# Optimization experiments

Hardware: AMD Instinct MI355X
Metric: run time of the kernel (lower is better)

The kernel has to match this reference:

```python
import jax, jax.numpy as jnp
import numpy as np

N, E, D, K, B = 50000, 600000, 128, 8, 64
E_DIM = 16  # edge_attr feature dim (hard-coded nn.Linear(16, in_dim))


def setup_inputs() -> dict:
    key = jax.random.key(0)
    ks = jax.random.split(key, 10)
    x = jax.random.normal(ks[0], (N, D), dtype=jnp.float32)
    edge_index = jax.random.randint(ks[1], (2, E), 0, N)
    edge_attr = jax.random.normal(ks[2], (E, E_DIM), dtype=jnp.float32)
    # binary pocket membership mask [N, K]
    pkt_mask = (jax.random.uniform(ks[3], (N, K)) < 0.3).astype(jnp.float32)
    batch = jnp.sort(jax.random.randint(ks[4], (N,), 0, B))
    s = 1.0 / np.sqrt(D)
    We = jax.random.normal(ks[5], (E_DIM, D), dtype=jnp.float32) * (1.0 / np.sqrt(E_DIM))
    be = jnp.zeros((D,), jnp.float32)
    W1 = jax.random.normal(ks[6], (D, D), dtype=jnp.float32) * s
    b1 = jnp.zeros((D,), jnp.float32)
    W2 = jax.random.normal(ks[7], (D, D), dtype=jnp.float32) * s
    b2 = jnp.zeros((D,), jnp.float32)
    eps = jnp.zeros((), jnp.float32)  # GINEConv train_eps init 0
    gamma = jnp.ones((D,), jnp.float32)
    beta = jnp.zeros((D,), jnp.float32)
    Wv = jax.random.normal(ks[8], (D, D), dtype=jnp.float32) * s
    bv = jnp.zeros((D,), jnp.float32)
    return {"x": x, "edge_index": edge_index, "edge_attr": edge_attr,
            "pkt_mask": pkt_mask, "batch": batch,
            "We": We, "be": be, "W1": W1, "b1": b1, "W2": W2, "b2": b2,
            "eps": eps, "gamma": gamma, "beta": beta, "Wv": Wv, "bv": bv}


def reference(x, edge_index, edge_attr, pkt_mask, batch,
              We, be, W1, b1, W2, b2, eps, gamma, beta, Wv, bv):
    src, dst = edge_index[0], edge_index[1]
    # edge_lin: [E,16] -> [E,D]
    edge_emb = edge_attr @ We + be
    # GINEConv: message = relu(x_src + edge_emb), scatter-add at dst
    msg = jax.nn.relu(x[src] + edge_emb)
    agg = jax.ops.segment_sum(msg, dst, num_segments=N)
    h = (1.0 + eps) * x + agg
    x_res = jax.nn.relu(h @ W1 + b1) @ W2 + b2  # nn MLP
    # virtual feedback: pocket-wise masked mean pooling per graph
    xw = x_res[:, None, :] * pkt_mask[:, :, None]          # [N,K,D]
    pocket_sum = jax.ops.segment_sum(xw.reshape(N, K * D), batch,
                                     num_segments=B).reshape(B, K, D)
    pocket_count = jax.ops.segment_sum(pkt_mask, batch, num_segments=B)  # [B,K]
    pocket_mean = pocket_sum / (pocket_count[:, :, None] + 1e-9)
    pocket_emb = pocket_mean @ Wv + bv                      # [B,K,D]
    node_pe = pocket_emb[batch]                             # gather -> [N,K,D]
    x_res = x_res + (node_pe * pkt_mask[:, :, None]).sum(axis=1)
    # LayerNorm (eps=1e-5, population variance as in torch)
    mu = x_res.mean(axis=-1, keepdims=True)
    var = ((x_res - mu) ** 2).mean(axis=-1, keepdims=True)
    y = (x_res - mu) / jnp.sqrt(var + 1e-5) * gamma + beta
    # ReLU activation; dropout is identity in eval mode
    return jax.nn.relu(y)
```

## Files before the change

kernel.cpp:

```cpp
#include <hip/hip_runtime.h>
#include <hip/hip_bf16.h>
#include <stdint.h>

#define D 128
#define K 8
#define BGRAPH 64
#define CH 64
#define GRP 4

typedef __attribute__((ext_vector_type(8))) short bf16x8;
typedef __attribute__((ext_vector_type(4))) float f32x4;
typedef __attribute__((ext_vector_type(2))) float f32x2;

__device__ __forceinline__ short f2bf(float f) {
    union { float f; uint32_t u; } v; v.f = f;
    const uint32_t r = (v.u + 0x7fffu + ((v.u >> 16) & 1u)) >> 16;
    return (short)r;
}
__device__ __forceinline__ float bflo(uint32_t u) {
    union { uint32_t u; float f; } v; v.u = u << 16; return v.f;
}
__device__ __forceinline__ float bfhi(uint32_t u) {
    union { uint32_t u; float f; } v; v.u = u & 0xffff0000u; return v.f;
}

__global__ __launch_bounds__(256) void prep_kernel(
    const float* __restrict__ x,
    const float* __restrict__ W1, const float* __restrict__ W2,
    const float* __restrict__ We, const float* __restrict__ be,
    const int* __restrict__ dst,
    __hip_bfloat16* __restrict__ xb,
    short* __restrict__ wb1t, short* __restrict__ wb2t,
    short* __restrict__ webt,
    int* __restrict__ deg,
    int NX, int E, int NBX, int NBW)
{
    const int b = blockIdx.x;
    const int t = threadIdx.x;
    if (b < NBX) {
        const int i = b * 2048 + t * 8;
        if (i + 8 <= NX) {
            const float4 a = *(const float4*)(x + i);
            const float4 c = *(const float4*)(x + i + 4);
            short v[8];
            v[0] = f2bf(a.x); v[1] = f2bf(a.y); v[2] = f2bf(a.z); v[3] = f2bf(a.w);
            v[4] = f2bf(c.x); v[5] = f2bf(c.y); v[6] = f2bf(c.z); v[7] = f2bf(c.w);
            *(uint4*)((short*)xb + i) = *(const uint4*)v;
        }
    } else if (b < NBX + NBW) {
        const int idx = (b - NBX) * 256 + t;
        if (idx < 2 * D * D) {
            const int which = idx >> 14;
            const int rem = idx & 16383;
            const int n = rem >> 7;
            const int k = rem & 127;
            const float* W = which ? W2 : W1;
            short* O = which ? wb2t : wb1t;
            O[n * D + k] = f2bf(W[(size_t)k * D + n]);
        } else {
            const int widx = idx - 2 * D * D;
            const int h = widx >> 12;
            const int c = (widx >> 5) & 127;
            const int k = widx & 31;
            float val = 0.f;
            if (k < 16) val = We[k * D + c];
            else if (k == 16) val = be[c];
            const short hi = f2bf(val);
            short outv;
            if (h == 0) outv = hi;
            else {
                union { uint32_t u; float f; } fh;
                fh.u = ((uint32_t)(unsigned short)hi) << 16;
                outv = f2bf(val - fh.f);
            }
            webt[(h << 12) + c * 32 + k] = outv;
        }
    } else {
        const int i = ((b - NBX - NBW) * 256 + t) * 4;
        if (i + 4 <= E) {
            const int4 v = *(const int4*)(dst + i);
            atomicAdd(&deg[v.x], 1);
            atomicAdd(&deg[v.y], 1);
            atomicAdd(&deg[v.z], 1);
            atomicAdd(&deg[v.w], 1);
        } else {
            for (int j = i; j < E; ++j) atomicAdd(&deg[dst[j]], 1);
        }
    }
}

__global__ __launch_bounds__(256) void scan_partial_kernel(
    const int* __restrict__ deg, int* __restrict__ bsum, int N)
{
    const int t = threadIdx.x;
    const int base = (blockIdx.x * 256 + t) * 4;
    int s = 0;
    if (base + 4 <= N) {
        const int4 v = *(const int4*)(deg + base);
        s = v.x + v.y + v.z + v.w;
    } else {
        for (int j = base; j < N; ++j) s += deg[j];
    }
    __shared__ int red[256];
    red[t] = s;
    __syncthreads();
    for (int off = 128; off; off >>= 1) {
        if (t < off) red[t] += red[t + off];
        __syncthreads();
    }
    if (t == 0) bsum[blockIdx.x] = red[0];
}

__global__ __launch_bounds__(64) void scan_top_kernel(
    const int* __restrict__ bsum, int* __restrict__ boffs, int nb)
{
    __shared__ int sh[64];
    const int t = threadIdx.x;
    const int v = (t < nb) ? bsum[t] : 0;
    sh[t] = v;
    __syncthreads();
    for (int off = 1; off < 64; off <<= 1) {
        const int u = (t >= off) ? sh[t - off] : 0;
        __syncthreads();
        sh[t] += u;
        __syncthreads();
    }
    if (t < nb) boffs[t] = sh[t] - v;
}

__global__ __launch_bounds__(256) void scan_final_kernel(
    const int* __restrict__ deg, const int* __restrict__ boffs,
    int* __restrict__ cursor, int N)
{
    const int t = threadIdx.x;
    const int base = (blockIdx.x * 256 + t) * 4;
    int v0 = 0, v1 = 0, v2 = 0, v3 = 0;
    if (base + 4 <= N) {
        const int4 v = *(const int4*)(deg + base);
        v0 = v.x; v1 = v.y; v2 = v.z; v3 = v.w;
    } else {
        if (base     < N) v0 = deg[base];
        if (base + 1 < N) v1 = deg[base + 1];
        if (base + 2 < N) v2 = deg[base + 2];
        if (base + 3 < N) v3 = deg[base + 3];
    }
    const int s = v0 + v1 + v2 + v3;
    __shared__ int sh[256];
    sh[t] = s;
    __syncthreads();
    for (int off = 1; off < 256; off <<= 1) {
        const int u = (t >= off) ? sh[t - off] : 0;
        __syncthreads();
        sh[t] += u;
        __syncthreads();
    }
    int ex = boffs[blockIdx.x] + sh[t] - s;
    if (base < N)     { cursor[base]     = ex; } ex += v0;
    if (base + 1 < N) { cursor[base + 1] = ex; } ex += v1;
    if (base + 2 < N) { cursor[base + 2] = ex; } ex += v2;
    if (base + 3 < N) { cursor[base + 3] = ex; }
}

__global__ __launch_bounds__(256) void scatter_kernel(
    const int* __restrict__ src, const int* __restrict__ dst,
    const float* __restrict__ ea,
    int* __restrict__ cursor, uint2* __restrict__ md,
    short* __restrict__ eabs, int E)
{
    const int i = blockIdx.x * 256 + threadIdx.x;
    if (i < E) {
        const unsigned sv = (unsigned)src[i];
        const unsigned dv = (unsigned)dst[i];
        const int p = atomicAdd(&cursor[dv], 1);
        md[p] = make_uint2(sv | (dv << 16), (unsigned)i);
        const float4* ep = (const float4*)(ea + (size_t)i * 16);
        const float4 a = ep[0], b = ep[1], c = ep[2], e4 = ep[3];
        short v[16];
        v[0]  = f2bf(a.x);  v[1]  = f2bf(a.y);  v[2]  = f2bf(a.z);  v[3]  = f2bf(a.w);
        v[4]  = f2bf(b.x);  v[5]  = f2bf(b.y);  v[6]  = f2bf(b.z);  v[7]  = f2bf(b.w);
        v[8]  = f2bf(c.x);  v[9]  = f2bf(c.y);  v[10] = f2bf(c.z);  v[11] = f2bf(c.w);
        v[12] = f2bf(e4.x); v[13] = f2bf(e4.y); v[14] = f2bf(e4.z); v[15] = f2bf(e4.w);
        uint4* op = (uint4*)(eabs + (size_t)p * 16);
        op[0] = *(const uint4*)v;
        op[1] = *(const uint4*)(v + 8);
    }
}

__device__ __forceinline__ void flush_row(
    float* __restrict__ agg, int node, int d, f32x2 acc, int first, int last)
{
    float* p = agg + (size_t)node * D + d;
    if (node == first || node == last) {
        if (acc.x != 0.f) atomicAdd(p,     acc.x);
        if (acc.y != 0.f) atomicAdd(p + 1, acc.y);
    } else {
        *(f32x2*)p = acc;
    }
}

__global__ __launch_bounds__(256) void gine_reduce_kernel(
    const __hip_bfloat16* __restrict__ xb, const uint2* __restrict__ md,
    const short* __restrict__ eabs, const short* __restrict__ webt,
    float* __restrict__ agg, int E)
{
    __shared__ float lsh[4][16 * 132];
    const int wave = threadIdx.x >> 6;
    const int lane = threadIdx.x & 63;
    const int chunk = __builtin_amdgcn_readfirstlane(blockIdx.x * 4 + wave);
    const int e0 = chunk * CH;
    if (e0 >= E) return;
    const int d = lane * 2;
    const int m = lane & 15;
    const int q = lane >> 4;
    float* myl = lsh[wave];
    const int NG = CH / GRP;

    bf16x8 bH[8], bL[8];
    #pragma unroll
    for (int ct = 0; ct < 8; ++ct) {
        bH[ct] = *(const bf16x8*)(webt +        (ct * 16 + m) * 32 + q * 8);
        bL[ct] = *(const bf16x8*)(webt + 4096 + (ct * 16 + m) * 32 + q * 8);
    }

    uint4 afcur = *(const uint4*)(eabs + (size_t)(e0 + m) * 16 + (q & 1) * 8);

    uint2 ma[GRP], mb[GRP], mc[GRP];
    #pragma unroll
    for (int j = 0; j < GRP; ++j) ma[j] = md[e0 + j];
    #pragma unroll
    for (int j = 0; j < GRP; ++j) mb[j] = md[e0 + GRP + j];
    #pragma unroll
    for (int j = 0; j < GRP; ++j) mc[j] = md[e0 + 2 * GRP + j];

    uint32_t xcur[GRP], xn1[GRP];
    #pragma unroll
    for (int j = 0; j < GRP; ++j)
        xcur[j] = *(const uint32_t*)(xb + (size_t)(ma[j].x & 0xffffu) * D + d);
    #pragma unroll
    for (int j = 0; j < GRP; ++j)
        xn1[j] = *(const uint32_t*)(xb + (size_t)(mb[j].x & 0xffffu) * D + d);

    const int first = (int)(ma[0].x >> 16);
    const int last  = (int)(md[e0 + CH - 1].x >> 16);

    f32x2 acc = {0.f, 0.f};
    int cur = first;

    for (int g = 0; g < NG; ++g) {
        if ((g & 3) == 0) {
            const int mg = g >> 2;
            uint4 afn = make_uint4(0u, 0u, 0u, 0u);
            if (mg < 3)
                afn = *(const uint4*)(eabs +
                    (size_t)(e0 + (mg + 1) * 16 + m) * 16 + (q & 1) * 8);
            uint4 au = afcur;
            if (q >= 2)
                au = make_uint4(q == 2 ? 0x3f80u : 0u, 0u, 0u, 0u);
            const bf16x8 a = *(const bf16x8*)&au;
            f32x4 mm[8];
            #pragma unroll
            for (int ct = 0; ct < 8; ++ct) {
                const f32x4 z = {0.f, 0.f, 0.f, 0.f};
                mm[ct] = __builtin_amdgcn_mfma_f32_16x16x32_bf16(a, bL[ct], z, 0, 0, 0);
            }
            #pragma unroll
            for (int ct = 0; ct < 8; ++ct)
                mm[ct] = __builtin_amdgcn_mfma_f32_16x16x32_bf16(a, bH[ct], mm[ct], 0, 0, 0);
            #pragma unroll
            for (int ct = 0; ct < 8; ++ct)
                #pragma unroll
                for (int r = 0; r < 4; ++r)
                    myl[(q * 4 + r) * 132 + ct * 16 + m] = mm[ct][r];
            afcur = afn;
        }

        uint2 mnn[GRP] = {};
        uint32_t xn2[GRP] = {};
        if (g + 3 < NG) {
            #pragma unroll
            for (int j = 0; j < GRP; ++j) mnn[j] = md[e0 + (g + 3) * GRP + j];
        }
        if (g + 2 < NG) {
            #pragma unroll
            for (int j = 0; j < GRP; ++j)
                xn2[j] = *(const uint32_t*)(xb + (size_t)(mc[j].x & 0xffffu) * D + d);
        }

        #pragma unroll
        for (int j = 0; j < GRP; ++j) {
            const int dk = (int)(ma[j].x >> 16);
            if (dk != cur) {
                flush_row(agg, cur, d, acc, first, last);
                acc.x = 0.f; acc.y = 0.f;
                cur = dk;
            }
            const uint32_t xu = xcur[j];
            const float2 em = *(const float2*)(myl + ((g & 3) * GRP + j) * 132 + d);
            const float v0 = em.x + bflo(xu);
            const float v1 = em.y + bfhi(xu);
            acc.x += v0 > 0.f ? v0 : 0.f;
            acc.y += v1 > 0.f ? v1 : 0.f;
        }

        #pragma unroll
        for (int j = 0; j < GRP; ++j) {
            ma[j] = mb[j]; mb[j] = mc[j]; mc[j] = mnn[j];
            xcur[j] = xn1[j]; xn1[j] = xn2[j];
        }
    }
    flush_row(agg, cur, d, acc, first, last);
}

#define MROWS 64
#define HSTR  132
__global__ __launch_bounds__(256) void mlp_mfma_kernel(
    const float* __restrict__ x, const float* __restrict__ agg,
    const float* __restrict__ epsp,
    const short* __restrict__ wb1t, const float* __restrict__ b1,
    const short* __restrict__ wb2t, const float* __restrict__ b2,
    float* __restrict__ xres, int N)
{
    __shared__ float hsh[MROWS * HSTR];
    const int row0 = blockIdx.x * MROWS;
    const float ep = 1.0f + epsp[0];

    for (int i = threadIdx.x; i < MROWS * D / 4; i += 256) {
        const int flat = i * 4;
        const int r = flat >> 7;
        const int c = flat & (D - 1);
        const int row = row0 + r;
        float4 hv = make_float4(0.f, 0.f, 0.f, 0.f);
        if (row < N) {
            const float4 xv = *(const float4*)(x   + (size_t)row * D + c);
            const float4 av = *(const float4*)(agg + (size_t)row * D + c);
            hv = make_float4(ep * xv.x + av.x, ep * xv.y + av.y,
                             ep * xv.z + av.z, ep * xv.w + av.w);
        }
        *(float4*)(hsh + r * HSTR + c) = hv;
    }
    __syncthreads();

    const int lane = threadIdx.x & 63;
    const int wrow = (threadIdx.x >> 6) * 16;
    const int m = lane & 15;
    const int q = lane >> 4;

    f32x4 acc[8];

    #pragma unroll
    for (int ct = 0; ct < 8; ++ct) {
        const float b = b1[ct * 16 + m];
        acc[ct] = (f32x4){b, b, b, b};
    }
    #pragma unroll
    for (int ks = 0; ks < 4; ++ks) {
        const float* ap = hsh + (wrow + m) * HSTR + ks * 32 + q * 8;
        float av[8];
        *(float4*)(av)     = *(const float4*)ap;
        *(float4*)(av + 4) = *(const float4*)(ap + 4);
        bf16x8 a;
        #pragma unroll
        for (int j = 0; j < 8; ++j) a[j] = f2bf(av[j]);
        #pragma unroll
        for (int ct = 0; ct < 8; ++ct) {
            const bf16x8 b = *(const bf16x8*)(wb1t + (ct * 16 + m) * D + ks * 32 + q * 8);
            acc[ct] = __builtin_amdgcn_mfma_f32_16x16x32_bf16(a, b, acc[ct], 0, 0, 0);
        }
    }
    #pragma unroll
    for (int ct = 0; ct < 8; ++ct)
        #pragma unroll
        for (int r = 0; r < 4; ++r) {
            const float v = acc[ct][r];
            hsh[(wrow + q * 4 + r) * HSTR + ct * 16 + m] = v > 0.f ? v : 0.f;
        }

    #pragma unroll
    for (int ct = 0; ct < 8; ++ct) {
        const float b = b2[ct * 16 + m];
        acc[ct] = (f32x4){b, b, b, b};
    }
    #pragma unroll
    for (int ks = 0; ks < 4; ++ks) {
        const float* ap = hsh + (wrow + m) * HSTR + ks * 32 + q * 8;
        float av[8];
        *(float4*)(av)     = *(const float4*)ap;
        *(float4*)(av + 4) = *(const float4*)(ap + 4);
        bf16x8 a;
        #pragma unroll
        for (int j = 0; j < 8; ++j) a[j] = f2bf(av[j]);
        #pragma unroll
        for (int ct = 0; ct < 8; ++ct) {
            const bf16x8 b = *(const bf16x8*)(wb2t + (ct * 16 + m) * D + ks * 32 + q * 8);
            acc[ct] = __builtin_amdgcn_mfma_f32_16x16x32_bf16(a, b, acc[ct], 0, 0, 0);
        }
    }
    #pragma unroll
    for (int r = 0; r < 4; ++r) {
        const int row = row0 + wrow + q * 4 + r;
        if (row < N) {
            #pragma unroll
            for (int ct = 0; ct < 8; ++ct)
                xres[(size_t)row * D + ct * 16 + m] = acc[ct][r];
        }
    }
}

#define PPARTS 32
__global__ __launch_bounds__(128) void pocket_sum_kernel(
    const float* __restrict__ xres, const float* __restrict__ pmask,
    const int* __restrict__ batch,
    float* __restrict__ psum, float* __restrict__ pcnt, int N)
{
    const int g = blockIdx.x / PPARTS;
    const int part = blockIdx.x % PPARTS;

    int lo, hi;
    {
        int l = 0, r = N;
        while (l < r) { int m = (l + r) >> 1; if (batch[m] < g) l = m + 1; else r = m; }
        lo = l;
        r = N;
        while (l < r) { int m = (l + r) >> 1; if (batch[m] < g + 1) l = m + 1; else r = m; }
        hi = l;
    }
    const int cnt = hi - lo;
    const int per = (cnt + PPARTS - 1) / PPARTS;
    const int s = lo + part * per;
    const int e = min(s + per, hi);

    const int d = threadIdx.x;
    float acc[K];
    #pragma unroll
    for (int k = 0; k < K; ++k) acc[k] = 0.0f;
    float c = 0.0f;

    for (int n = s; n < e; ++n) {
        const float xv = xres[(size_t)n * D + d];
        const float4 m0 = *(const float4*)(pmask + (size_t)n * K);
        const float4 m1 = *(const float4*)(pmask + (size_t)n * K + 4);
        acc[0] += m0.x * xv; acc[1] += m0.y * xv;
        acc[2] += m0.z * xv; acc[3] += m0.w * xv;
        acc[4] += m1.x * xv; acc[5] += m1.y * xv;
        acc[6] += m1.z * xv; acc[7] += m1.w * xv;
        if (d < K) c += pmask[(size_t)n * K + d];
    }
    #pragma unroll
    for (int k = 0; k < K; ++k)
        atomicAdd(&psum[(size_t)g * (K * D) + k * D + d], acc[k]);
    if (d < K) atomicAdd(&pcnt[g * K + d], c);
}

__global__ __launch_bounds__(128) void pocket_emb_kernel(
    const float* __restrict__ psum, const float* __restrict__ pcnt,
    const float* __restrict__ Wv, const float* __restrict__ bv,
    float* __restrict__ pemb)
{
    __shared__ float smean[K * D];
    __shared__ float scnt[K];
    const int g = blockIdx.x;
    const int d = threadIdx.x;
    if (d < K) scnt[d] = pcnt[g * K + d];
    __syncthreads();
    #pragma unroll
    for (int k = 0; k < K; ++k)
        smean[k * D + d] = psum[(size_t)g * (K * D) + k * D + d] / (scnt[k] + 1e-9f);
    __syncthreads();

    float acc[K];
    const float bvv = bv[d];
    #pragma unroll
    for (int k = 0; k < K; ++k) acc[k] = bvv;
    for (int j = 0; j < D; ++j) {
        const float w = Wv[j * D + d];
        #pragma unroll
        for (int k = 0; k < K; ++k) acc[k] += smean[k * D + j] * w;
    }
    #pragma unroll
    for (int k = 0; k < K; ++k)
        pemb[(size_t)g * (K * D) + k * D + d] = acc[k];
}

__global__ __launch_bounds__(256) void ln_kernel(
    const float* __restrict__ xres, const float* __restrict__ pmask,
    const int* __restrict__ batch, const float* __restrict__ pemb,
    const float* __restrict__ gamma, const float* __restrict__ beta,
    float* __restrict__ out, int N)
{
    const int wave = threadIdx.x >> 6;
    const int lane = threadIdx.x & 63;
    const int n = blockIdx.x * 4 + wave;
    if (n >= N) return;
    const int d = lane * 2;

    float2 v = *(const float2*)(xres + (size_t)n * D + d);
    const int g = batch[n];
    const float* pe = pemb + (size_t)g * (K * D);
    const float4 m0 = *(const float4*)(pmask + (size_t)n * K);
    const float4 m1 = *(const float4*)(pmask + (size_t)n * K + 4);
    const float mk[K] = {m0.x, m0.y, m0.z, m0.w, m1.x, m1.y, m1.z, m1.w};
    #pragma unroll
    for (int k = 0; k < K; ++k) {
        if (mk[k] != 0.0f) {
            const float2 p = *(const float2*)(pe + k * D + d);
            v.x += mk[k] * p.x;
            v.y += mk[k] * p.y;
        }
    }

    float s = v.x + v.y;
    #pragma unroll
    for (int off = 32; off; off >>= 1) s += __shfl_xor(s, off, 64);
    const float mu = s * (1.0f / 128.0f);
    const float d0 = v.x - mu, d1 = v.y - mu;
    float sq = d0 * d0 + d1 * d1;
    #pragma unroll
    for (int off = 32; off; off >>= 1) sq += __shfl_xor(sq, off, 64);
    const float var = sq * (1.0f / 128.0f);
    const float inv = rsqrtf(var + 1e-5f);

    const float2 gm = *(const float2*)(gamma + d);
    const float2 bt = *(const float2*)(beta + d);
    float y0 = d0 * inv * gm.x + bt.x;
    float y1 = d1 * inv * gm.y + bt.y;
    y0 = y0 > 0.0f ? y0 : 0.0f;
    y1 = y1 > 0.0f ? y1 : 0.0f;
    *(float2*)(out + (size_t)n * D + d) = make_float2(y0, y1);
}

extern "C" void kernel_launch(void* const* d_in, const int* in_sizes, int n_in,
                              void* d_out, int out_size, void* d_ws, size_t ws_size,
                              hipStream_t stream)
{
    const float* x     = (const float*)d_in[0];
    const int*   ei    = (const int*)  d_in[1];
    const float* ea    = (const float*)d_in[2];
    const float* pmask = (const float*)d_in[3];
    const int*   batch = (const int*)  d_in[4];
    const float* We    = (const float*)d_in[5];
    const float* be    = (const float*)d_in[6];
    const float* W1    = (const float*)d_in[7];
    const float* b1    = (const float*)d_in[8];
    const float* W2    = (const float*)d_in[9];
    const float* b2    = (const float*)d_in[10];
    const float* epsp  = (const float*)d_in[11];
    const float* gamma = (const float*)d_in[12];
    const float* beta  = (const float*)d_in[13];
    const float* Wv    = (const float*)d_in[14];
    const float* bv    = (const float*)d_in[15];
    float* out = (float*)d_out;

    const int N = in_sizes[0] / D;
    const int E = in_sizes[1] / 2;
    const int* src = ei;
    const int* dst = ei + E;

    int*   deg  = (int*)d_ws;
    float* agg  = (float*)(deg + N);
    float* psum = agg + (size_t)N * D;
    float* pcnt = psum + (size_t)BGRAPH * K * D;
    float* xres = pcnt + (size_t)BGRAPH * K;
    float* pemb = xres + (size_t)N * D;
    float* extra = pemb + (size_t)BGRAPH * K * D;
    __hip_bfloat16* xb = (__hip_bfloat16*)(extra + 128);
    short* wb1t = (short*)(xb + (size_t)N * D);
    short* wb2t = wb1t + (size_t)D * D;
    short* webt = wb2t + (size_t)D * D;

    int*   cursor = (int*)xres;
    uint2* md  = (uint2*)(((uintptr_t)(cursor + N) + 15) & ~(uintptr_t)15);
    short* eabs = (short*)(md + E);

    int*  bsum  = (int*)extra;
    int*  boffs = bsum + 64;

    const int nb = (N + 1023) / 1024;
    const int nchunks = (E + CH - 1) / CH;
    const int NX = N * D;
    const int NBX = NX / 2048;
    const int NBW = (2 * D * D + 2 * 128 * 32) / 256;
    const int NBH = (E / 4 + 255) / 256;

    const size_t zero_bytes =
        ((size_t)N + (size_t)N * D + (size_t)BGRAPH * K * D + BGRAPH * K) * sizeof(float);
    hipMemsetAsync(d_ws, 0, zero_bytes, stream);

    prep_kernel<<<NBX + NBW + NBH, 256, 0, stream>>>(
        x, W1, W2, We, be, dst, xb, wb1t, wb2t, webt, deg,
        NX, E, NBX, NBW);
    scan_partial_kernel<<<nb, 256, 0, stream>>>(deg, bsum, N);
    scan_top_kernel<<<1, 64, 0, stream>>>(bsum, boffs, nb);
    scan_final_kernel<<<nb, 256, 0, stream>>>(deg, boffs, cursor, N);
    scatter_kernel<<<(E + 255) / 256, 256, 0, stream>>>(
        src, dst, ea, cursor, md, eabs, E);
    gine_reduce_kernel<<<(nchunks + 3) / 4, 256, 0, stream>>>(
        xb, md, eabs, webt, agg, E);

    mlp_mfma_kernel<<<(N + MROWS - 1) / MROWS, 256, 0, stream>>>(
        x, agg, epsp, wb1t, b1, wb2t, b2, xres, N);
    pocket_sum_kernel<<<BGRAPH * PPARTS, 128, 0, stream>>>(
        xres, pmask, batch, psum, pcnt, N);
    pocket_emb_kernel<<<BGRAPH, 128, 0, stream>>>(psum, pcnt, Wv, bv, pemb);
    ln_kernel<<<(N + 3) / 4, 256, 0, stream>>>(
        xres, pmask, batch, pemb, gamma, beta, out, N);
}
```

Measured before the change: 349.4 us.

## Collapse three-kernel degree scan into one block; fuse agg zeroing into scatter

Replaces the three-kernel hierarchical prefix scan over node degrees with a single 1024-thread block, where each thread sums a contiguous range serially. It also moves the zeroing of the N×D aggregation buffer out of the memset and into the scatter kernel as a grid-stride loop, reordering the workspace so the memset covers only the small buffers. The aim is to cut kernel launches and a separate memset pass. In exchange, the single-block scan is serial per thread with uncoalesced strided reads, and the scatter kernel takes on extra store traffic.

Measured after the change: 413.6 us. 18.4% more time.

```diff
diff --git a/kernel.cpp b/kernel.cpp
--- a/kernel.cpp
+++ b/kernel.cpp
@@ -89,85 +89,39 @@
     }
 }
 
-__global__ __launch_bounds__(256) void scan_partial_kernel(
-    const int* __restrict__ deg, int* __restrict__ bsum, int N)
-{
+__global__ __launch_bounds__(1024) void scan_kernel(
+    const int* __restrict__ deg, int* __restrict__ cursor, int N)
+{
+    __shared__ int sh[1024];
     const int t = threadIdx.x;
-    const int base = (blockIdx.x * 256 + t) * 4;
+    const int per = (N + 1023) >> 10;
+    const int s0 = t * per;
+    const int e0 = min(s0 + per, N);
     int s = 0;
-    if (base + 4 <= N) {
-        const int4 v = *(const int4*)(deg + base);
-        s = v.x + v.y + v.z + v.w;
-    } else {
-        for (int j = base; j < N; ++j) s += deg[j];
-    }
-    __shared__ int red[256];
-    red[t] = s;
+    for (int j = s0; j < e0; ++j) s += deg[j];
+    sh[t] = s;
     __syncthreads();
-    for (int off = 128; off; off >>= 1) {
-        if (t < off) red[t] += red[t + off];
-        __syncthreads();
-    }
-    if (t == 0) bsum[blockIdx.x] = red[0];
-}
-
-__global__ __launch_bounds__(64) void scan_top_kernel(
-    const int* __restrict__ bsum, int* __restrict__ boffs, int nb)
-{
-    __shared__ int sh[64];
-    const int t = threadIdx.x;
-    const int v = (t < nb) ? bsum[t] : 0;
-    sh[t] = v;
-    __syncthreads();
-    for (int off = 1; off < 64; off <<= 1) {
+    for (int off = 1; off < 1024; off <<= 1) {
         const int u = (t >= off) ? sh[t - off] : 0;
         __syncthreads();
         sh[t] += u;
         __syncthreads();
     }
-    if (t < nb) boffs[t] = sh[t] - v;
-}
-
-__global__ __launch_bounds__(256) void scan_final_kernel(
-    const int* __restrict__ deg, const int* __restrict__ boffs,
-    int* __restrict__ cursor, int N)
-{
-    const int t = threadIdx.x;
-    const int base = (blockIdx.x * 256 + t) * 4;
-    int v0 = 0, v1 = 0, v2 = 0, v3 = 0;
-    if (base + 4 <= N) {
-        const int4 v = *(const int4*)(deg + base);
-        v0 = v.x; v1 = v.y; v2 = v.z; v3 = v.w;
-    } else {
-        if (base     < N) v0 = deg[base];
-        if (base + 1 < N) v1 = deg[base + 1];
-        if (base + 2 < N) v2 = deg[base + 2];
-        if (base + 3 < N) v3 = deg[base + 3];
-    }
-    const int s = v0 + v1 + v2 + v3;
-    __shared__ int sh[256];
-    sh[t] = s;
-    __syncthreads();
-    for (int off = 1; off < 256; off <<= 1) {
-        const int u = (t >= off) ? sh[t - off] : 0;
-        __syncthreads();
-        sh[t] += u;
-        __syncthreads();
-    }
-    int ex = boffs[blockIdx.x] + sh[t] - s;
-    if (base < N)     { cursor[base]     = ex; } ex += v0;
-    if (base + 1 < N) { cursor[base + 1] = ex; } ex += v1;
-    if (base + 2 < N) { cursor[base + 2] = ex; } ex += v2;
-    if (base + 3 < N) { cursor[base + 3] = ex; }
+    int ex = sh[t] - s;
+    for (int j = s0; j < e0; ++j) { cursor[j] = ex; ex += deg[j]; }
 }
 
 __global__ __launch_bounds__(256) void scatter_kernel(
     const int* __restrict__ src, const int* __restrict__ dst,
     const float* __restrict__ ea,
     int* __restrict__ cursor, uint2* __restrict__ md,
-    short* __restrict__ eabs, int E)
+    short* __restrict__ eabs, float* __restrict__ agg, int E, int NXD)
 {
     const int i = blockIdx.x * 256 + threadIdx.x;
+    const int stride = gridDim.x * 256;
+    for (size_t z = (size_t)i * 4; z < (size_t)NXD; z += (size_t)stride * 4)
+        *(float4*)(agg + z) = make_float4(0.f, 0.f, 0.f, 0.f);
+
     if (i < E) {
         const unsigned sv = (unsigned)src[i];
         const unsigned dv = (unsigned)dst[i];
@@ -556,10 +510,10 @@
     const int* dst = ei + E;
 
     int*   deg  = (int*)d_ws;
-    float* agg  = (float*)(deg + N);
-    float* psum = agg + (size_t)N * D;
+    float* psum = (float*)(deg + N);
     float* pcnt = psum + (size_t)BGRAPH * K * D;
-    float* xres = pcnt + (size_t)BGRAPH * K;
+    float* agg  = pcnt + (size_t)BGRAPH * K;
+    float* xres = agg + (size_t)N * D;
     float* pemb = xres + (size_t)N * D;
     float* extra = pemb + (size_t)BGRAPH * K * D;
     __hip_bfloat16* xb = (__hip_bfloat16*)(extra + 128);
@@ -571,28 +525,23 @@
     uint2* md  = (uint2*)(((uintptr_t)(cursor + N) + 15) & ~(uintptr_t)15);
     short* eabs = (short*)(md + E);
 
-    int*  bsum  = (int*)extra;
-    int*  boffs = bsum + 64;
-
-    const int nb = (N + 1023) / 1024;
     const int nchunks = (E + CH - 1) / CH;
     const int NX = N * D;
     const int NBX = NX / 2048;
     const int NBW = (2 * D * D + 2 * 128 * 32) / 256;
     const int NBH = (E / 4 + 255) / 256;
+    const int NSC = (E + 255) / 256;
 
     const size_t zero_bytes =
-        ((size_t)N + (size_t)N * D + (size_t)BGRAPH * K * D + BGRAPH * K) * sizeof(float);
+        ((size_t)N + (size_t)BGRAPH * K * D + BGRAPH * K) * sizeof(float);
     hipMemsetAsync(d_ws, 0, zero_bytes, stream);
 
     prep_kernel<<<NBX + NBW + NBH, 256, 0, stream>>>(
         x, W1, W2, We, be, dst, xb, wb1t, wb2t, webt, deg,
         NX, E, NBX, NBW);
-    scan_partial_kernel<<<nb, 256, 0, stream>>>(deg, bsum, N);
-    scan_top_kernel<<<1, 64, 0, stream>>>(bsum, boffs, nb);
-    scan_final_kernel<<<nb, 256, 0, stream>>>(deg, boffs, cursor, N);
-    scatter_kernel<<<(E + 255) / 256, 256, 0, stream>>>(
-        src, dst, ea, cursor, md, eabs, E);
+    scan_kernel<<<1, 1024, 0, stream>>>(deg, cursor, N);
+    scatter_kernel<<<NSC, 256, 0, stream>>>(
+        src, dst, ea, cursor, md, eabs, agg, E, NX);
     gine_reduce_kernel<<<(nchunks + 3) / 4, 256, 0, stream>>>(
         xb, md, eabs, webt, agg, E);
 
```

## Fuse pocket masked-sum into MLP epilogue and merge scan top into final scan

Applied to the files above, without the earlier changes.

The pocket-wise masked sum is now computed inside the MLP kernel's epilogue. Each block stages its 64 output rows in shared memory, reduces them per pocket and graph, and issues atomics to psum/pcnt, so the separate pocket_sum kernel no longer rereads xres. The top-level prefix scan over block sums is also folded into each scan_final block, removing one small launch. This saves a launch and a full pass over xres, at the cost of more global atomics (about 782 blocks × 8 × 128) and extra epilogue work and shared-memory pressure in the MLP kernel.

New measurement: 368.7 us. 5.5% more time.

```diff
diff --git a/kernel.cpp b/kernel.cpp
--- a/kernel.cpp
+++ b/kernel.cpp
@@ -111,28 +111,26 @@
     if (t == 0) bsum[blockIdx.x] = red[0];
 }
 
-__global__ __launch_bounds__(64) void scan_top_kernel(
-    const int* __restrict__ bsum, int* __restrict__ boffs, int nb)
-{
-    __shared__ int sh[64];
+__global__ __launch_bounds__(256) void scan_final_kernel(
+    const int* __restrict__ deg, const int* __restrict__ bsum,
+    int* __restrict__ cursor, int N, int nb)
+{
+    __shared__ int topsh[64];
+    __shared__ int sh[256];
     const int t = threadIdx.x;
-    const int v = (t < nb) ? bsum[t] : 0;
-    sh[t] = v;
+
+    const int own = bsum[blockIdx.x];
+    if (t < 64) topsh[t] = (t < nb) ? bsum[t] : 0;
     __syncthreads();
     for (int off = 1; off < 64; off <<= 1) {
-        const int u = (t >= off) ? sh[t - off] : 0;
+        int u = 0;
+        if (t < 64 && t >= off) u = topsh[t - off];
         __syncthreads();
-        sh[t] += u;
+        if (t < 64) topsh[t] += u;
         __syncthreads();
     }
-    if (t < nb) boffs[t] = sh[t] - v;
-}
-
-__global__ __launch_bounds__(256) void scan_final_kernel(
-    const int* __restrict__ deg, const int* __restrict__ boffs,
-    int* __restrict__ cursor, int N)
-{
-    const int t = threadIdx.x;
+    const int extop = topsh[blockIdx.x] - own;
+
     const int base = (blockIdx.x * 256 + t) * 4;
     int v0 = 0, v1 = 0, v2 = 0, v3 = 0;
     if (base + 4 <= N) {
@@ -145,7 +143,6 @@
         if (base + 3 < N) v3 = deg[base + 3];
     }
     const int s = v0 + v1 + v2 + v3;
-    __shared__ int sh[256];
     sh[t] = s;
     __syncthreads();
     for (int off = 1; off < 256; off <<= 1) {
@@ -154,7 +151,7 @@
         sh[t] += u;
         __syncthreads();
     }
-    int ex = boffs[blockIdx.x] + sh[t] - s;
+    int ex = extop + sh[t] - s;
     if (base < N)     { cursor[base]     = ex; } ex += v0;
     if (base + 1 < N) { cursor[base + 1] = ex; } ex += v1;
     if (base + 2 < N) { cursor[base + 2] = ex; } ex += v2;
@@ -318,9 +315,14 @@
     const float* __restrict__ epsp,
     const short* __restrict__ wb1t, const float* __restrict__ b1,
     const short* __restrict__ wb2t, const float* __restrict__ b2,
-    float* __restrict__ xres, int N)
+    const float* __restrict__ pmask, const int* __restrict__ batch,
+    float* __restrict__ xres, float* __restrict__ psum,
+    float* __restrict__ pcnt, int N)
 {
     __shared__ float hsh[MROWS * HSTR];
+    __shared__ float pmsh[MROWS][K];
+    __shared__ int   bsh[MROWS];
+    __shared__ float pcl[2][K];
     const int row0 = blockIdx.x * MROWS;
     const float ep = 1.0f + epsp[0];
 
@@ -338,10 +340,24 @@
         }
         *(float4*)(hsh + r * HSTR + c) = hv;
     }
+    for (int i = threadIdx.x; i < MROWS; i += 256) {
+        const int row = row0 + i;
+        if (row < N) {
+            bsh[i] = batch[row];
+            *(float4*)&pmsh[i][0] = *(const float4*)(pmask + (size_t)row * K);
+            *(float4*)&pmsh[i][4] = *(const float4*)(pmask + (size_t)row * K + 4);
+        } else {
+            bsh[i] = -1;
+            *(float4*)&pmsh[i][0] = make_float4(0.f, 0.f, 0.f, 0.f);
+            *(float4*)&pmsh[i][4] = make_float4(0.f, 0.f, 0.f, 0.f);
+        }
+    }
+    if (threadIdx.x < 2 * K) ((float*)pcl)[threadIdx.x] = 0.f;
     __syncthreads();
 
     const int lane = threadIdx.x & 63;
-    const int wrow = (threadIdx.x >> 6) * 16;
+    const int wv   = threadIdx.x >> 6;
+    const int wrow = wv * 16;
     const int m = lane & 15;
     const int q = lane >> 4;
 
@@ -395,60 +411,68 @@
             acc[ct] = __builtin_amdgcn_mfma_f32_16x16x32_bf16(a, b, acc[ct], 0, 0, 0);
         }
     }
+    __syncthreads();
     #pragma unroll
     for (int r = 0; r < 4; ++r) {
         const int row = row0 + wrow + q * 4 + r;
-        if (row < N) {
-            #pragma unroll
-            for (int ct = 0; ct < 8; ++ct)
-                xres[(size_t)row * D + ct * 16 + m] = acc[ct][r];
-        }
-    }
-}
-
-#define PPARTS 32
-__global__ __launch_bounds__(128) void pocket_sum_kernel(
-    const float* __restrict__ xres, const float* __restrict__ pmask,
-    const int* __restrict__ batch,
-    float* __restrict__ psum, float* __restrict__ pcnt, int N)
-{
-    const int g = blockIdx.x / PPARTS;
-    const int part = blockIdx.x % PPARTS;
-
-    int lo, hi;
-    {
-        int l = 0, r = N;
-        while (l < r) { int m = (l + r) >> 1; if (batch[m] < g) l = m + 1; else r = m; }
-        lo = l;
-        r = N;
-        while (l < r) { int m = (l + r) >> 1; if (batch[m] < g + 1) l = m + 1; else r = m; }
-        hi = l;
-    }
-    const int cnt = hi - lo;
-    const int per = (cnt + PPARTS - 1) / PPARTS;
-    const int s = lo + part * per;
-    const int e = min(s + per, hi);
-
-    const int d = threadIdx.x;
-    float acc[K];
-    #pragma unroll
-    for (int k = 0; k < K; ++k) acc[k] = 0.0f;
-    float c = 0.0f;
-
-    for (int n = s; n < e; ++n) {
-        const float xv = xres[(size_t)n * D + d];
-        const float4 m0 = *(const float4*)(pmask + (size_t)n * K);
-        const float4 m1 = *(const float4*)(pmask + (size_t)n * K + 4);
-        acc[0] += m0.x * xv; acc[1] += m0.y * xv;
-        acc[2] += m0.z * xv; acc[3] += m0.w * xv;
-        acc[4] += m1.x * xv; acc[5] += m1.y * xv;
-        acc[6] += m1.z * xv; acc[7] += m1.w * xv;
-        if (d < K) c += pmask[(size_t)n * K + d];
-    }
-    #pragma unroll
-    for (int k = 0; k < K; ++k)
-        atomicAdd(&psum[(size_t)g * (K * D) + k * D + d], acc[k]);
-    if (d < K) atomicAdd(&pcnt[g * K + d], c);
+        #pragma unroll
+        for (int ct = 0; ct < 8; ++ct) {
+            const float v = acc[ct][r];
+            hsh[(wrow + q * 4 + r) * HSTR + ct * 16 + m] = v;
+            if (row < N) xres[(size_t)row * D + ct * 16 + m] = v;
+        }
+    }
+    __syncthreads();
+
+    const int lastr = min(MROWS - 1, N - 1 - row0);
+    const int g0 = bsh[0];
+    const int g1 = bsh[lastr];
+
+    #pragma unroll
+    for (int kk = 0; kk < 2; ++kk) {
+        const int k = wv * 2 + kk;
+        #pragma unroll
+        for (int half = 0; half < 2; ++half) {
+            const int col = lane + 64 * half;
+            float s0 = 0.f, s1 = 0.f;
+            for (int row = 0; row < MROWS; ++row) {
+                const float w = pmsh[row][k];
+                if (w != 0.f) {
+                    const float v = hsh[row * HSTR + col];
+                    const int gr = bsh[row];
+                    if (gr == g0)       s0 += w * v;
+                    else if (gr == g1)  s1 += w * v;
+                    else atomicAdd(&psum[(size_t)gr * (K * D) + k * D + col], w * v);
+                }
+            }
+            if (s0 != 0.f)
+                atomicAdd(&psum[(size_t)g0 * (K * D) + k * D + col], s0);
+            if (g1 != g0 && s1 != 0.f)
+                atomicAdd(&psum[(size_t)g1 * (K * D) + k * D + col], s1);
+        }
+    }
+
+    if (wv == 0) {
+        const int gr = bsh[lane];
+        #pragma unroll
+        for (int k = 0; k < K; ++k) {
+            const float w = pmsh[lane][k];
+            if (w != 0.f) {
+                if (gr == g0)      atomicAdd(&pcl[0][k], w);
+                else if (gr == g1) atomicAdd(&pcl[1][k], w);
+                else               atomicAdd(&pcnt[gr * K + k], w);
+            }
+        }
+    }
+    __syncthreads();
+    if (threadIdx.x < K) {
+        const float v = pcl[0][threadIdx.x];
+        if (v != 0.f) atomicAdd(&pcnt[g0 * K + threadIdx.x], v);
+    } else if (threadIdx.x < 2 * K) {
+        const int k = threadIdx.x - K;
+        const float v = pcl[1][k];
+        if (g1 != g0 && v != 0.f) atomicAdd(&pcnt[g1 * K + k], v);
+    }
 }
 
 __global__ __launch_bounds__(128) void pocket_emb_kernel(
@@ -572,7 +596,6 @@
     short* eabs = (short*)(md + E);
 
     int*  bsum  = (int*)extra;
-    int*  boffs = bsum + 64;
 
     const int nb = (N + 1023) / 1024;
     const int nchunks = (E + CH - 1) / CH;
@@ -589,17 +612,15 @@
         x, W1, W2, We, be, dst, xb, wb1t, wb2t, webt, deg,
         NX, E, NBX, NBW);
     scan_partial_kernel<<<nb, 256, 0, stream>>>(deg, bsum, N);
-    scan_top_kernel<<<1, 64, 0, stream>>>(bsum, boffs, nb);
-    scan_final_kernel<<<nb, 256, 0, stream>>>(deg, boffs, cursor, N);
+    scan_final_kernel<<<nb, 256, 0, stream>>>(deg, bsum, cursor, N, nb);
     scatter_kernel<<<(E + 255) / 256, 256, 0, stream>>>(
         src, dst, ea, cursor, md, eabs, E);
     gine_reduce_kernel<<<(nchunks + 3) / 4, 256, 0, stream>>>(
         xb, md, eabs, webt, agg, E);
 
     mlp_mfma_kernel<<<(N + MROWS - 1) / MROWS, 256, 0, stream>>>(
-        x, agg, epsp, wb1t, b1, wb2t, b2, xres, N);
-    pocket_sum_kernel<<<BGRAPH * PPARTS, 128, 0, stream>>>(
-        xres, pmask, batch, psum, pcnt, N);
+        x, agg, epsp, wb1t, b1, wb2t, b2, pmask, batch,
+        xres, psum, pcnt, N);
     pocket_emb_kernel<<<BGRAPH, 128, 0, stream>>>(psum, pcnt, Wv, bv, pemb);
     ln_kernel<<<(N + 3) / 4, 256, 0, stream>>>(
         xres, pmask, batch, pemb, gamma, beta, out, N);
```
